# Kernel optimization log

Hardware: AMD Instinct MI355X
Metric: run time of the kernel (lower is better)

## Reference

```python
import jax, jax.numpy as jnp
import numpy as np

D_KEY = 128
INF = 1e9  # stands in for the module's global INF constant


def setup_inputs() -> dict:
    key = jax.random.key(0)
    kq, kk, kv = jax.random.split(key, 3)
    B, S, D = 8, 4096, D_KEY
    return {
        "query": jax.random.normal(kq, (B, S, D), dtype=jnp.float32),
        "keys": jax.random.normal(kk, (B, S, D), dtype=jnp.float32),
        "values": jax.random.normal(kv, (B, S, D), dtype=jnp.float32),
    }


def reference(query, keys, values):
    # dot_products: [B, Sq, Sk]
    scores = jnp.einsum("bqd,bkd->bqk", query, keys)
    S = scores.shape[-1]
    # causal: subtract INF on strict upper triangle (triu(1)), applied BEFORE scaling
    causal = jnp.triu(jnp.ones((S, S), dtype=scores.dtype), 1) * INF
    logits = (scores - causal[None, :, :]) / jnp.asarray(np.sqrt(D_KEY), scores.dtype)
    # legacy F.softmax on 3D transposed tensor == softmax over key axis
    probs = jax.nn.softmax(logits, axis=-1)
    # dropout with p=0.0 is identity
    return jnp.einsum("bqk,bkd->bqd", probs, values)
```

## Files before the change

kernel.cpp:

```cpp
#include <hip/hip_runtime.h>

#define B_SZ   8
#define S_LEN  4096
#define D_K    128
#define KB     64
#define CH     16
#define NCHUNK 640

#define PT_STR 72

typedef short  short8  __attribute__((ext_vector_type(8)));
typedef float  floatx4 __attribute__((ext_vector_type(4)));

#define EXP2F(x) exp2f(x)

__device__ __forceinline__ unsigned bfround(float x) {
  unsigned u = __builtin_bit_cast(unsigned, x);
  return (u + 0x7fffu + ((u >> 16) & 1u)) >> 16;
}
__device__ __forceinline__ unsigned bfpack2(float a, float b) {
  return bfround(a) | (bfround(b) << 16);
}
__device__ __forceinline__ unsigned cvtpk(float lo, float hi) {
  unsigned r;
  asm("v_cvt_pk_bf16_f32 %0, %1, %2" : "=v"(r) : "v"(lo), "v"(hi));
  return r;
}


__device__ __forceinline__ void dma16(const void* g, const void* l) {
  __builtin_amdgcn_global_load_lds(
      (__attribute__((address_space(1))) unsigned int*)(unsigned long long)g,
      (__attribute__((address_space(3))) unsigned int*)(unsigned int)(unsigned long long)l,
      16, 0, 0);
}


__global__ __launch_bounds__(256)
void prep(const float* __restrict__ K, const float* __restrict__ V,
          unsigned short* __restrict__ Kb, unsigned short* __restrict__ Vt,
          int* __restrict__ cnt) {
  __shared__ float tile[64][129];
  const int tid = threadIdx.x;
  const int bid = blockIdx.x;
  if (bid == 0 && tid == 0) *cnt = 0;
  const int b   = bid >> 6;
  const int s   = bid & 63;
  const int kt  = s * 64;

  {
    const int r  = tid >> 2;
    const int cq = tid & 3;
    const float* kp = K + (size_t)(b * S_LEN + kt + r) * D_K + cq * 32;
    unsigned short* kdst = Kb + (size_t)bid * 8192 + r * 128;
    const int xr = (r & 7) << 4;
#pragma unroll
    for (int jj = 0; jj < 4; ++jj) {
      float4 f0 = *(const float4*)(kp + jj * 8);
      float4 f1 = *(const float4*)(kp + jj * 8 + 4);
      uint4 u;
      u.x = bfpack2(f0.x, f0.y);
      u.y = bfpack2(f0.z, f0.w);
      u.z = bfpack2(f1.x, f1.y);
      u.w = bfpack2(f1.z, f1.w);
      const int o = (cq * 64 + jj * 16) ^ xr;
      *(uint4*)(kdst + (o >> 1)) = u;
    }
  }

  {
    const int k  = tid >> 2;
    const int cq = tid & 3;
    const float* vp = V + (size_t)(b * S_LEN + kt + k) * D_K + cq * 32;
#pragma unroll
    for (int i = 0; i < 8; ++i) {
      float4 f = *(const float4*)(vp + i * 4);
      tile[k][cq * 32 + i * 4]     = f.x;
      tile[k][cq * 32 + i * 4 + 1] = f.y;
      tile[k][cq * 32 + i * 4 + 2] = f.z;
      tile[k][cq * 32 + i * 4 + 3] = f.w;
    }
  }
  __syncthreads();

  {
    const int d = tid >> 1;
    const int h = tid & 1;
    unsigned short* vdst = Vt + (size_t)bid * 8192 + d * 64;
    const int xr = (d & 7) << 4;
#pragma unroll
    for (int jj = 0; jj < 4; ++jj) {
      const int k0 = h * 32 + jj * 8;
      uint4 u;
      u.x = bfpack2(tile[k0 + 0][d], tile[k0 + 1][d]);
      u.y = bfpack2(tile[k0 + 2][d], tile[k0 + 3][d]);
      u.z = bfpack2(tile[k0 + 4][d], tile[k0 + 5][d]);
      u.w = bfpack2(tile[k0 + 6][d], tile[k0 + 7][d]);
      const int o = (h * 64 + jj * 16) ^ xr;
      *(uint4*)(vdst + (o >> 1)) = u;
    }
  }
}


__global__ __launch_bounds__(256, 2)
void attn_worker(const float* __restrict__ Q, const unsigned short* __restrict__ Kb,
                 const unsigned short* __restrict__ Vt, int* __restrict__ cnt,
                 float* __restrict__ ml, float* __restrict__ pO) {
  __shared__ __align__(16) short Klds[2][8192];
  __shared__ __align__(16) short Vtlds[2][8192];
  __shared__ __align__(16) short Plds[4 * 16 * PT_STR];
  __shared__ int s_chunk;

  const int tid  = threadIdx.x;
  const int lane = tid & 63;
  const int w    = tid >> 6;
  const int l15  = lane & 15;
  const int quad = lane >> 4;
  const int xk   = (l15 & 7) << 3;

  const float CSC = 0.12752041f;

  for (;;) {
    if (tid == 0) s_chunk = atomicAdd(cnt, 1);
    __syncthreads();
    const int c = s_chunk;
    if (c >= NCHUNK) break;

    int b, q, j;
    if (c < 416) {
      const int r = c >> 3;  b = c & 7;
      if      (r <  4) { q = 31;              j = r;         }
      else if (r < 28) { q = 30 - (r-4)/3;    j = (r-4)%3;   }
      else if (r < 44) { q = 22 - (r-28)/2;   j = (r-28)%2;  }
      else             { q = 14 - (r-44);     j = 0;         }
    } else {
      const int rc = c - 416;
      const int g  = rc >> 5;
      const int t  = rc & 31;
      b = t & 7;
      q = (6 - g) + 8 * (3 - (t >> 3));
      j = (q + 1) >> 3;
    }

    const int q0 = q * 128;
    const int s0 = j * CH;
    const int s1 = min(s0 + CH, 2 * q + 2);

    short8 bq[2][4];
    int qg[2];
#pragma unroll
    for (int sub = 0; sub < 2; ++sub) {
      qg[sub] = q0 + w * 32 + sub * 16 + l15;
      const float* qrow = Q + (size_t)(b * S_LEN + qg[sub]) * D_K + quad * 8;
#pragma unroll
      for (int kd = 0; kd < 4; ++kd) {
        float4 f0 = *(const float4*)(qrow + kd * 32);
        float4 f1 = *(const float4*)(qrow + kd * 32 + 4);
        union { short8 s; unsigned u[4]; } t;
        t.u[0] = bfpack2(f0.x, f0.y);
        t.u[1] = bfpack2(f0.z, f0.w);
        t.u[2] = bfpack2(f1.x, f1.y);
        t.u[3] = bfpack2(f1.z, f1.w);
        bq[sub][kd] = t.s;
      }
    }

    floatx4 acc[2][8];
#pragma unroll
    for (int sub = 0; sub < 2; ++sub)
#pragma unroll
      for (int nc = 0; nc < 8; ++nc) acc[sub][nc] = (floatx4){0.f, 0.f, 0.f, 0.f};
    float m_run[2] = {-1e30f, -1e30f}, l_run[2] = {0.f, 0.f};

    const unsigned short* kb0 = Kb + (size_t)b * 64 * 8192;
    const unsigned short* vb0 = Vt + (size_t)b * 64 * 8192;
    const int lo = lane * 8;

#define STAGE(BUF, S)                                                          \
    do {                                                                       \
      const unsigned short* kg_ = kb0 + (size_t)(S) * 8192 + w * 2048 + lo;    \
      const unsigned short* vg_ = vb0 + (size_t)(S) * 8192 + w * 2048 + lo;    \
      short* kl_ = &Klds[BUF][w * 2048];                                       \
      short* vl_ = &Vtlds[BUF][w * 2048];                                      \
      _Pragma("unroll")                                                        \
      for (int i_ = 0; i_ < 4; ++i_) dma16(kg_ + i_ * 512, kl_ + i_ * 512);    \
      _Pragma("unroll")                                                        \
      for (int i_ = 0; i_ < 4; ++i_) dma16(vg_ + i_ * 512, vl_ + i_ * 512);    \
    } while (0)

    STAGE(s0 & 1, s0);
    if (s0 + 1 < s1) {
      STAGE((s0 + 1) & 1, s0 + 1);
      asm volatile("s_waitcnt vmcnt(8)" ::: "memory");
    } else {
      asm volatile("s_waitcnt vmcnt(0)" ::: "memory");
    }
    __builtin_amdgcn_s_barrier();
    __builtin_amdgcn_sched_barrier(0);

    for (int s = s0; s < s1; ++s) {
      const int kt  = s * KB;
      const int cur = s & 1;
      const short* Kl = &Klds[cur][0];
      const short* Vl = &Vtlds[cur][0];
      const bool act = (kt <= q0 + w * 32 + 31);

      short8 pa[2][2];
      if (act) {
        floatx4 st[2][4];
        __builtin_amdgcn_s_setprio(1);
#pragma unroll
        for (int kf = 0; kf < 4; ++kf) {
          floatx4 c0 = (floatx4){0.f, 0.f, 0.f, 0.f};
          floatx4 c1 = (floatx4){0.f, 0.f, 0.f, 0.f};
#pragma unroll
          for (int kd = 0; kd < 4; ++kd) {
            short8 a = *(const short8*)(&Kl[((kf * 16 + l15) << 7) + ((kd * 32 + quad * 8) ^ xk)]);
            c0 = __builtin_amdgcn_mfma_f32_16x16x32_bf16(a, bq[0][kd], c0, 0, 0, 0);
            c1 = __builtin_amdgcn_mfma_f32_16x16x32_bf16(a, bq[1][kd], c1, 0, 0, 0);
          }
          st[0][kf] = c0;
          st[1][kf] = c1;
        }
        __builtin_amdgcn_s_setprio(0);

#pragma unroll
        for (int sub = 0; sub < 2; ++sub) {
          if (kt + 63 > q0 + w * 32 + sub * 16) {
#pragma unroll
            for (int kf = 0; kf < 4; ++kf)
#pragma unroll
              for (int r = 0; r < 4; ++r) {
                int key = kt + kf * 16 + quad * 4 + r;
                if (key > qg[sub]) st[sub][kf][r] = -1e30f;
              }
          }
        }

#pragma unroll
        for (int sub = 0; sub < 2; ++sub) {
          float mx = st[sub][0][0];
#pragma unroll
          for (int kf = 0; kf < 4; ++kf)
#pragma unroll
            for (int r = 0; r < 4; ++r) mx = fmaxf(mx, st[sub][kf][r]);
          mx = fmaxf(mx, __shfl_xor(mx, 16, 64));
          mx = fmaxf(mx, __shfl_xor(mx, 32, 64));
          const float m_new = fmaxf(m_run[sub], mx);
          const bool  grow  = __any(m_new > m_run[sub]);

          float p[4][4];
          float tsum = 0.f;
#pragma unroll
          for (int kf = 0; kf < 4; ++kf)
#pragma unroll
            for (int r = 0; r < 4; ++r) {
              p[kf][r] = EXP2F((st[sub][kf][r] - m_new) * CSC);
              tsum += p[kf][r];
            }
          tsum += __shfl_xor(tsum, 16, 64);
          tsum += __shfl_xor(tsum, 32, 64);

          if (grow) {
            const float alpha = EXP2F((m_run[sub] - m_new) * CSC);
            l_run[sub] = l_run[sub] * alpha + tsum;
#pragma unroll
            for (int r = 0; r < 4; ++r) {
              const float ar = __shfl(alpha, quad * 4 + r, 64);
#pragma unroll
              for (int nc = 0; nc < 8; ++nc) acc[sub][nc][r] *= ar;
            }
          } else {
            l_run[sub] = l_run[sub] + tsum;
          }
          m_run[sub] = m_new;

          short* pw = &Plds[(w * 16 + l15) * PT_STR];
#pragma unroll
          for (int kf = 0; kf < 4; ++kf) {
            uint2 u;
            u.x = cvtpk(p[kf][0], p[kf][1]);
            u.y = cvtpk(p[kf][2], p[kf][3]);
            *(uint2*)(&pw[kf * 16 + quad * 4]) = u;
          }
          __asm__ __volatile__("" ::: "memory");
          pa[sub][0] = *(const short8*)(&pw[quad * 8]);
          pa[sub][1] = *(const short8*)(&pw[32 + quad * 8]);
          __asm__ __volatile__("" ::: "memory");
        }

        __builtin_amdgcn_s_setprio(1);
#pragma unroll
        for (int nc = 0; nc < 8; ++nc) {
          short8 bv0 = *(const short8*)(&Vl[((nc * 16 + l15) << 6) + ((quad * 8) ^ xk)]);
          short8 bv1 = *(const short8*)(&Vl[((nc * 16 + l15) << 6) + ((32 + quad * 8) ^ xk)]);
          acc[0][nc] = __builtin_amdgcn_mfma_f32_16x16x32_bf16(pa[0][0], bv0, acc[0][nc], 0, 0, 0);
          acc[0][nc] = __builtin_amdgcn_mfma_f32_16x16x32_bf16(pa[0][1], bv1, acc[0][nc], 0, 0, 0);
          acc[1][nc] = __builtin_amdgcn_mfma_f32_16x16x32_bf16(pa[1][0], bv0, acc[1][nc], 0, 0, 0);
          acc[1][nc] = __builtin_amdgcn_mfma_f32_16x16x32_bf16(pa[1][1], bv1, acc[1][nc], 0, 0, 0);
        }
        __builtin_amdgcn_s_setprio(0);
      }

      asm volatile("s_waitcnt lgkmcnt(0)" ::: "memory");
      __builtin_amdgcn_s_barrier();
      __builtin_amdgcn_sched_barrier(0);
      if (s + 2 < s1) {
        STAGE(cur, s + 2);
        asm volatile("s_waitcnt vmcnt(8)" ::: "memory");
      } else if (s + 1 < s1) {
        asm volatile("s_waitcnt vmcnt(0)" ::: "memory");
      }
      __builtin_amdgcn_s_barrier();
      __builtin_amdgcn_sched_barrier(0);
    }
#undef STAGE

    const int slot = ((b << 5) | q) * 4 + j;
    float* po = pO + (size_t)slot * 16384;
#pragma unroll
    for (int sub = 0; sub < 2; ++sub) {
#pragma unroll
      for (int r = 0; r < 4; ++r) {
        const int qrow = w * 32 + sub * 16 + quad * 4 + r;
        float* op = po + qrow * D_K + l15;
#pragma unroll
        for (int nc = 0; nc < 8; ++nc) op[nc * 16] = acc[sub][nc][r];
      }
      if (quad == 0) {
        const int qrow = w * 32 + sub * 16 + l15;
        ml[(size_t)slot * 256 + qrow * 2]     = m_run[sub];
        ml[(size_t)slot * 256 + qrow * 2 + 1] = l_run[sub];
      }
    }
  }
}


__global__ __launch_bounds__(256)
void attn_combine(const float* __restrict__ ml, const float* __restrict__ pO,
                  float* __restrict__ O) {
  const int t = blockIdx.x;
  const int b = t >> 5;
  const int q = t & 31;
  const int ncb = (2 * q + 17) >> 4;
  const float CSC = 0.12752041f;

  const int tid = threadIdx.x;
  const int ql  = tid >> 1;
  const int dh  = (tid & 1) * 64;

  float m[4], l[4], wgt[4];
  float M = -1e30f;
#pragma unroll
  for (int jj = 0; jj < 4; ++jj) {
    if (jj < ncb) {
      const int slot = t * 4 + jj;
      m[jj] = ml[(size_t)slot * 256 + ql * 2];
      l[jj] = ml[(size_t)slot * 256 + ql * 2 + 1];
      M = fmaxf(M, m[jj]);
    }
  }
  float L = 0.f;
#pragma unroll
  for (int jj = 0; jj < 4; ++jj)
    if (jj < ncb) { wgt[jj] = EXP2F((m[jj] - M) * CSC); L += wgt[jj] * l[jj]; }
  const float inv = 1.0f / L;

  float4 out[16];
#pragma unroll
  for (int v = 0; v < 16; ++v) out[v] = make_float4(0.f, 0.f, 0.f, 0.f);
#pragma unroll
  for (int jj = 0; jj < 4; ++jj) {
    if (jj < ncb) {
      const float* src = pO + (size_t)(t * 4 + jj) * 16384 + ql * D_K + dh;
      const float wj = wgt[jj];
#pragma unroll
      for (int v = 0; v < 16; ++v) {
        float4 f = *(const float4*)(src + v * 4);
        out[v].x += wj * f.x;  out[v].y += wj * f.y;
        out[v].z += wj * f.z;  out[v].w += wj * f.w;
      }
    }
  }
  float* dst = O + ((size_t)(b * S_LEN) + q * 128 + ql) * D_K + dh;
#pragma unroll
  for (int v = 0; v < 16; ++v) {
    *(float4*)(dst + v * 4) = make_float4(out[v].x * inv, out[v].y * inv,
                                          out[v].z * inv, out[v].w * inv);
  }
}


#define KT_STR 136
#define VT_STR 72

__global__ __launch_bounds__(256, 2)
void attn_fwd_fb(const float* __restrict__ Q, const float* __restrict__ K,
                 const float* __restrict__ V, float* __restrict__ O) {
  __shared__ __align__(16) short Klds[KB * KT_STR];
  __shared__ __align__(16) short Vtlds[D_K * VT_STR];
  __shared__ __align__(16) short Plds[4 * 16 * PT_STR];

  const int tid  = threadIdx.x;
  const int lane = tid & 63;
  const int w    = tid >> 6;
  const int l15  = lane & 15;
  const int quad = lane >> 4;

  const int bid = blockIdx.x;
  const int b   = bid & 7;
  const int qi  = 63 - (bid >> 3);
  const int q0  = qi * 64;

  const float CSC = 0.12752041f;

  const int    qg   = q0 + w * 16 + l15;
  const float* qrow = Q + (size_t)(b * S_LEN + qg) * D_K + quad * 8;
  short8 bq[4];
#pragma unroll
  for (int kd = 0; kd < 4; ++kd) {
    float4 f0 = *(const float4*)(qrow + kd * 32);
    float4 f1 = *(const float4*)(qrow + kd * 32 + 4);
    union { short8 s; unsigned u[4]; } t;
    t.u[0] = bfpack2(f0.x, f0.y);
    t.u[1] = bfpack2(f0.z, f0.w);
    t.u[2] = bfpack2(f1.x, f1.y);
    t.u[3] = bfpack2(f1.z, f1.w);
    bq[kd] = t.s;
  }

  floatx4 acc[8];
#pragma unroll
  for (int nc = 0; nc < 8; ++nc) acc[nc] = (floatx4){0.f, 0.f, 0.f, 0.f};
  float m_run = -1e30f, l_run = 0.f;

  const int d4 = tid & 31;
  const int kq = tid >> 5;
  const int nsteps = qi + 1;

  for (int s = 0; s < nsteps; ++s) {
    const int kt = s * KB;
#pragma unroll
    for (int r2 = 0; r2 < 2; ++r2) {
      const int row = r2 * 32 + kq * 4;
      const float* kp = K + (size_t)(b * S_LEN + kt + row) * D_K + d4 * 4;
      const float* vp = V + (size_t)(b * S_LEN + kt + row) * D_K + d4 * 4;
      float4 fk[4], fv[4];
#pragma unroll
      for (int i = 0; i < 4; ++i) {
        fk[i] = *(const float4*)(kp + i * D_K);
        fv[i] = *(const float4*)(vp + i * D_K);
      }
#pragma unroll
      for (int i = 0; i < 4; ++i) {
        uint2 u;
        u.x = bfpack2(fk[i].x, fk[i].y);
        u.y = bfpack2(fk[i].z, fk[i].w);
        *(uint2*)(&Klds[(row + i) * KT_STR + d4 * 4]) = u;
      }
#pragma unroll
      for (int c = 0; c < 4; ++c) {
        float e0 = ((const float*)&fv[0])[c];
        float e1 = ((const float*)&fv[1])[c];
        float e2 = ((const float*)&fv[2])[c];
        float e3 = ((const float*)&fv[3])[c];
        uint2 u;
        u.x = bfpack2(e0, e1);
        u.y = bfpack2(e2, e3);
        *(uint2*)(&Vtlds[(d4 * 4 + c) * VT_STR + row]) = u;
      }
    }
    __syncthreads();

    floatx4 st[4];
#pragma unroll
    for (int kf = 0; kf < 4; ++kf) {
      floatx4 cc = (floatx4){0.f, 0.f, 0.f, 0.f};
#pragma unroll
      for (int kd = 0; kd < 4; ++kd) {
        short8 a = *(const short8*)(&Klds[(kf * 16 + l15) * KT_STR + kd * 32 + quad * 8]);
        cc = __builtin_amdgcn_mfma_f32_16x16x32_bf16(a, bq[kd], cc, 0, 0, 0);
      }
      st[kf] = cc;
    }

    if (s == nsteps - 1) {
#pragma unroll
      for (int kf = 0; kf < 4; ++kf)
#pragma unroll
        for (int rr = 0; rr < 4; ++rr) {
          int key = kt + kf * 16 + quad * 4 + rr;
          if (key > qg) st[kf][rr] = -1e30f;
        }
    }

    float mx = st[0][0];
#pragma unroll
    for (int kf = 0; kf < 4; ++kf)
#pragma unroll
      for (int rr = 0; rr < 4; ++rr) mx = fmaxf(mx, st[kf][rr]);
    mx = fmaxf(mx, __shfl_xor(mx, 16, 64));
    mx = fmaxf(mx, __shfl_xor(mx, 32, 64));
    const float m_new = fmaxf(m_run, mx);
    const float alpha = EXP2F((m_run - m_new) * CSC);

    float p[4][4];
    float tsum = 0.f;
#pragma unroll
    for (int kf = 0; kf < 4; ++kf)
#pragma unroll
      for (int rr = 0; rr < 4; ++rr) {
        p[kf][rr] = EXP2F((st[kf][rr] - m_new) * CSC);
        tsum += p[kf][rr];
      }
    tsum += __shfl_xor(tsum, 16, 64);
    tsum += __shfl_xor(tsum, 32, 64);
    l_run = l_run * alpha + tsum;
    m_run = m_new;

#pragma unroll
    for (int rr = 0; rr < 4; ++rr) {
      const float ar = __shfl(alpha, quad * 4 + rr, 64);
#pragma unroll
      for (int nc = 0; nc < 8; ++nc) acc[nc][rr] *= ar;
    }

    short* pw = &Plds[(w * 16 + l15) * PT_STR];
#pragma unroll
    for (int kf = 0; kf < 4; ++kf) {
      uint2 u;
      u.x = bfpack2(p[kf][0], p[kf][1]);
      u.y = bfpack2(p[kf][2], p[kf][3]);
      *(uint2*)(&pw[kf * 16 + quad * 4]) = u;
    }
    __asm__ __volatile__("" ::: "memory");
    short8 pa0 = *(const short8*)(&pw[quad * 8]);
    short8 pa1 = *(const short8*)(&pw[32 + quad * 8]);

#pragma unroll
    for (int nc = 0; nc < 8; ++nc) {
      short8 bv0 = *(const short8*)(&Vtlds[(nc * 16 + l15) * VT_STR + quad * 8]);
      acc[nc] = __builtin_amdgcn_mfma_f32_16x16x32_bf16(pa0, bv0, acc[nc], 0, 0, 0);
      short8 bv1 = *(const short8*)(&Vtlds[(nc * 16 + l15) * VT_STR + 32 + quad * 8]);
      acc[nc] = __builtin_amdgcn_mfma_f32_16x16x32_bf16(pa1, bv1, acc[nc], 0, 0, 0);
    }
    __syncthreads();
  }

#pragma unroll
  for (int rr = 0; rr < 4; ++rr) {
    const float lr  = __shfl(l_run, quad * 4 + rr, 64);
    const float inv = 1.0f / lr;
    const int qout  = q0 + w * 16 + quad * 4 + rr;
    float* op = O + (size_t)(b * S_LEN + qout) * D_K + l15;
#pragma unroll
    for (int nc = 0; nc < 8; ++nc) op[nc * 16] = acc[nc][rr] * inv;
  }
}


extern "C" void kernel_launch(void* const* d_in, const int* in_sizes, int n_in,
                              void* d_out, int out_size, void* d_ws, size_t ws_size,
                              hipStream_t stream) {
  const float* Q = (const float*)d_in[0];
  const float* K = (const float*)d_in[1];
  const float* V = (const float*)d_in[2];
  float* O = (float*)d_out;

  const size_t elems = (size_t)B_SZ * S_LEN * D_K;

  const size_t off_ml = 256;
  const size_t off_po = off_ml + 1024ull * 256 * 4;
  const size_t off_kb = off_po + 1024ull * 16384 * 4;
  const size_t off_vt = off_kb + elems * 2;
  const size_t need   = off_vt + elems * 2;

  if (ws_size >= need) {
    char* ws = (char*)d_ws;
    int*            cnt = (int*)ws;
    float*          mlp = (float*)(ws + off_ml);
    float*          po  = (float*)(ws + off_po);
    unsigned short* Kbp = (unsigned short*)(ws + off_kb);
    unsigned short* Vtp = (unsigned short*)(ws + off_vt);

    prep<<<dim3(B_SZ * 64), dim3(256), 0, stream>>>(K, V, Kbp, Vtp, cnt);
    attn_worker<<<dim3(512), dim3(256), 0, stream>>>(Q, Kbp, Vtp, cnt, mlp, po);
    attn_combine<<<dim3(256), dim3(256), 0, stream>>>(mlp, po, O);
  } else {
    attn_fwd_fb<<<dim3(512), dim3(256), 0, stream>>>(Q, K, V, O);
  }
}
```

Baseline: 181.3 us.

## Replace atomic work queue with static 256-row 8-wave chunk schedule

Drops the persistent atomic-counter work loop and launches one 512-thread block per statically mapped chunk of 256 query rows by up to 8 key tiles, with balancing partial chunks for even tiles. The P staging buffer now reuses the current K LDS buffer after a barrier, which frees shared memory so more blocks can be resident. The combine kernel is rewritten for the new slot layout with up to 8 partials. This removes atomic and queue overhead and shares K/V staging across more query rows, at the cost of relying on a fixed schedule, which may balance less well, and adding an extra barrier per tile.

Measured after the change: 377.5 us. +108.2%, slower.

```diff
diff --git a/kernel.cpp b/kernel.cpp
--- a/kernel.cpp
+++ b/kernel.cpp
@@ -4,10 +4,8 @@
 #define S_LEN  4096
 #define D_K    128
 #define KB     64
-#define CH     16
-#define NCHUNK 640
-
-#define PT_STR 72
+#define NFULL  512
+#define NCHUNK 576
 
 typedef short  short8  __attribute__((ext_vector_type(8)));
 typedef float  floatx4 __attribute__((ext_vector_type(4)));
@@ -38,12 +36,10 @@
 
 __global__ __launch_bounds__(256)
 void prep(const float* __restrict__ K, const float* __restrict__ V,
-          unsigned short* __restrict__ Kb, unsigned short* __restrict__ Vt,
-          int* __restrict__ cnt) {
+          unsigned short* __restrict__ Kb, unsigned short* __restrict__ Vt) {
   __shared__ float tile[64][129];
   const int tid = threadIdx.x;
   const int bid = blockIdx.x;
-  if (bid == 0 && tid == 0) *cnt = 0;
   const int b   = bid >> 6;
   const int s   = bid & 63;
   const int kt  = s * 64;
@@ -103,14 +99,12 @@
 }
 
 
-__global__ __launch_bounds__(256, 2)
+__global__ __launch_bounds__(512, 4)
 void attn_worker(const float* __restrict__ Q, const unsigned short* __restrict__ Kb,
-                 const unsigned short* __restrict__ Vt, int* __restrict__ cnt,
+                 const unsigned short* __restrict__ Vt,
                  float* __restrict__ ml, float* __restrict__ pO) {
   __shared__ __align__(16) short Klds[2][8192];
   __shared__ __align__(16) short Vtlds[2][8192];
-  __shared__ __align__(16) short Plds[4 * 16 * PT_STR];
-  __shared__ int s_chunk;
 
   const int tid  = threadIdx.x;
   const int lane = tid & 63;
@@ -121,218 +115,211 @@
 
   const float CSC = 0.12752041f;
 
-  for (;;) {
-    if (tid == 0) s_chunk = atomicAdd(cnt, 1);
-    __syncthreads();
-    const int c = s_chunk;
-    if (c >= NCHUNK) break;
-
-    int b, q, j;
-    if (c < 416) {
-      const int r = c >> 3;  b = c & 7;
-      if      (r <  4) { q = 31;              j = r;         }
-      else if (r < 28) { q = 30 - (r-4)/3;    j = (r-4)%3;   }
-      else if (r < 44) { q = 22 - (r-28)/2;   j = (r-28)%2;  }
-      else             { q = 14 - (r-44);     j = 0;         }
-    } else {
-      const int rc = c - 416;
-      const int g  = rc >> 5;
-      const int t  = rc & 31;
-      b = t & 7;
-      q = (6 - g) + 8 * (3 - (t >> 3));
-      j = (q + 1) >> 3;
-    }
-
-    const int q0 = q * 128;
-    const int s0 = j * CH;
-    const int s1 = min(s0 + CH, 2 * q + 2);
-
-    short8 bq[2][4];
-    int qg[2];
-#pragma unroll
-    for (int sub = 0; sub < 2; ++sub) {
-      qg[sub] = q0 + w * 32 + sub * 16 + l15;
-      const float* qrow = Q + (size_t)(b * S_LEN + qg[sub]) * D_K + quad * 8;
-#pragma unroll
-      for (int kd = 0; kd < 4; ++kd) {
-        float4 f0 = *(const float4*)(qrow + kd * 32);
-        float4 f1 = *(const float4*)(qrow + kd * 32 + 4);
-        union { short8 s; unsigned u[4]; } t;
-        t.u[0] = bfpack2(f0.x, f0.y);
-        t.u[1] = bfpack2(f0.z, f0.w);
-        t.u[2] = bfpack2(f1.x, f1.y);
-        t.u[3] = bfpack2(f1.z, f1.w);
-        bq[sub][kd] = t.s;
-      }
-    }
-
-    floatx4 acc[2][8];
-#pragma unroll
-    for (int sub = 0; sub < 2; ++sub)
-#pragma unroll
-      for (int nc = 0; nc < 8; ++nc) acc[sub][nc] = (floatx4){0.f, 0.f, 0.f, 0.f};
-    float m_run[2] = {-1e30f, -1e30f}, l_run[2] = {0.f, 0.f};
-
-    const unsigned short* kb0 = Kb + (size_t)b * 64 * 8192;
-    const unsigned short* vb0 = Vt + (size_t)b * 64 * 8192;
-    const int lo = lane * 8;
+  const int orig = blockIdx.x;
+  const int wid  = (orig & 7) * 72 + (orig >> 3);
+
+  int b, t, s0, s1;
+  if (wid < NFULL) {
+    b = wid >> 6;
+    int r = wid & 63;
+    t = 15;
+    while (r >= ((t + 1) >> 1)) { r -= (t + 1) >> 1; --t; }
+    s0 = r * 8;  s1 = s0 + 8;
+  } else {
+    const int rc = wid - NFULL;
+    b = rc >> 3;
+    t = 14 - 2 * (rc & 7);
+    s0 = 4 * t;  s1 = s0 + 4;
+  }
+  const int q0 = t << 8;
+
+  short8 bq[2][4];
+  int qg[2];
+#pragma unroll
+  for (int sub = 0; sub < 2; ++sub) {
+    qg[sub] = q0 + w * 32 + sub * 16 + l15;
+    const float* qrow = Q + (size_t)(b * S_LEN + qg[sub]) * D_K + quad * 8;
+#pragma unroll
+    for (int kd = 0; kd < 4; ++kd) {
+      float4 f0 = *(const float4*)(qrow + kd * 32);
+      float4 f1 = *(const float4*)(qrow + kd * 32 + 4);
+      union { short8 s; unsigned u[4]; } tt;
+      tt.u[0] = bfpack2(f0.x, f0.y);
+      tt.u[1] = bfpack2(f0.z, f0.w);
+      tt.u[2] = bfpack2(f1.x, f1.y);
+      tt.u[3] = bfpack2(f1.z, f1.w);
+      bq[sub][kd] = tt.s;
+    }
+  }
+
+  floatx4 acc[2][8];
+#pragma unroll
+  for (int sub = 0; sub < 2; ++sub)
+#pragma unroll
+    for (int nc = 0; nc < 8; ++nc) acc[sub][nc] = (floatx4){0.f, 0.f, 0.f, 0.f};
+  float m_run[2] = {-1e30f, -1e30f}, l_run[2] = {0.f, 0.f};
+
+  const unsigned short* kb0 = Kb + (size_t)b * 64 * 8192;
+  const unsigned short* vb0 = Vt + (size_t)b * 64 * 8192;
+  const int lo = lane * 8;
 
 #define STAGE(BUF, S)                                                          \
-    do {                                                                       \
-      const unsigned short* kg_ = kb0 + (size_t)(S) * 8192 + w * 2048 + lo;    \
-      const unsigned short* vg_ = vb0 + (size_t)(S) * 8192 + w * 2048 + lo;    \
-      short* kl_ = &Klds[BUF][w * 2048];                                       \
-      short* vl_ = &Vtlds[BUF][w * 2048];                                      \
-      _Pragma("unroll")                                                        \
-      for (int i_ = 0; i_ < 4; ++i_) dma16(kg_ + i_ * 512, kl_ + i_ * 512);    \
-      _Pragma("unroll")                                                        \
-      for (int i_ = 0; i_ < 4; ++i_) dma16(vg_ + i_ * 512, vl_ + i_ * 512);    \
-    } while (0)
-
-    STAGE(s0 & 1, s0);
-    if (s0 + 1 < s1) {
-      STAGE((s0 + 1) & 1, s0 + 1);
-      asm volatile("s_waitcnt vmcnt(8)" ::: "memory");
-    } else {
-      asm volatile("s_waitcnt vmcnt(0)" ::: "memory");
-    }
+  do {                                                                         \
+    const unsigned short* kg_ = kb0 + (size_t)(S) * 8192 + w * 1024 + lo;      \
+    const unsigned short* vg_ = vb0 + (size_t)(S) * 8192 + w * 1024 + lo;      \
+    short* kl_ = &Klds[BUF][w * 1024];                                         \
+    short* vl_ = &Vtlds[BUF][w * 1024];                                        \
+    dma16(kg_, kl_);        dma16(kg_ + 512, kl_ + 512);                       \
+    dma16(vg_, vl_);        dma16(vg_ + 512, vl_ + 512);                       \
+  } while (0)
+
+  STAGE(s0 & 1, s0);
+  if (s0 + 1 < s1) {
+    STAGE((s0 + 1) & 1, s0 + 1);
+    asm volatile("s_waitcnt vmcnt(4)" ::: "memory");
+  } else {
+    asm volatile("s_waitcnt vmcnt(0)" ::: "memory");
+  }
+  __builtin_amdgcn_s_barrier();
+  __builtin_amdgcn_sched_barrier(0);
+
+  for (int s = s0; s < s1; ++s) {
+    const int kt  = s * KB;
+    const int cur = s & 1;
+    const short* Kl = &Klds[cur][0];
+    const short* Vl = &Vtlds[cur][0];
+    const bool act = (kt <= q0 + w * 32 + 31);
+
+    floatx4 st[2][4];
+    if (act) {
+      __builtin_amdgcn_s_setprio(1);
+#pragma unroll
+      for (int kf = 0; kf < 4; ++kf) {
+        floatx4 c0 = (floatx4){0.f, 0.f, 0.f, 0.f};
+        floatx4 c1 = (floatx4){0.f, 0.f, 0.f, 0.f};
+#pragma unroll
+        for (int kd = 0; kd < 4; ++kd) {
+          short8 a = *(const short8*)(&Kl[((kf * 16 + l15) << 7) + ((kd * 32 + quad * 8) ^ xk)]);
+          c0 = __builtin_amdgcn_mfma_f32_16x16x32_bf16(a, bq[0][kd], c0, 0, 0, 0);
+          c1 = __builtin_amdgcn_mfma_f32_16x16x32_bf16(a, bq[1][kd], c1, 0, 0, 0);
+        }
+        st[0][kf] = c0;
+        st[1][kf] = c1;
+      }
+      __builtin_amdgcn_s_setprio(0);
+
+#pragma unroll
+      for (int sub = 0; sub < 2; ++sub) {
+        if (kt + 63 > q0 + w * 32 + sub * 16) {
+#pragma unroll
+          for (int kf = 0; kf < 4; ++kf)
+#pragma unroll
+            for (int r = 0; r < 4; ++r) {
+              int key = kt + kf * 16 + quad * 4 + r;
+              if (key > qg[sub]) st[sub][kf][r] = -1e30f;
+            }
+        }
+      }
+    }
+
     __builtin_amdgcn_s_barrier();
     __builtin_amdgcn_sched_barrier(0);
 
-    for (int s = s0; s < s1; ++s) {
-      const int kt  = s * KB;
-      const int cur = s & 1;
-      const short* Kl = &Klds[cur][0];
-      const short* Vl = &Vtlds[cur][0];
-      const bool act = (kt <= q0 + w * 32 + 31);
-
-      short8 pa[2][2];
-      if (act) {
-        floatx4 st[2][4];
-        __builtin_amdgcn_s_setprio(1);
+    short8 pa[2][2];
+    if (act) {
+      short* pw = &Klds[cur][(w * 16 + l15) << 6];
+#pragma unroll
+      for (int sub = 0; sub < 2; ++sub) {
+        float mx = st[sub][0][0];
+#pragma unroll
+        for (int kf = 0; kf < 4; ++kf)
+#pragma unroll
+          for (int r = 0; r < 4; ++r) mx = fmaxf(mx, st[sub][kf][r]);
+        mx = fmaxf(mx, __shfl_xor(mx, 16, 64));
+        mx = fmaxf(mx, __shfl_xor(mx, 32, 64));
+        const float m_new = fmaxf(m_run[sub], mx);
+        const bool  grow  = __any(m_new > m_run[sub]);
+
+        float p[4][4];
+        float tsum = 0.f;
+#pragma unroll
+        for (int kf = 0; kf < 4; ++kf)
+#pragma unroll
+          for (int r = 0; r < 4; ++r) {
+            p[kf][r] = EXP2F((st[sub][kf][r] - m_new) * CSC);
+            tsum += p[kf][r];
+          }
+        tsum += __shfl_xor(tsum, 16, 64);
+        tsum += __shfl_xor(tsum, 32, 64);
+
+        if (grow) {
+          const float alpha = EXP2F((m_run[sub] - m_new) * CSC);
+          l_run[sub] = l_run[sub] * alpha + tsum;
+#pragma unroll
+          for (int r = 0; r < 4; ++r) {
+            const float ar = __shfl(alpha, quad * 4 + r, 64);
+#pragma unroll
+            for (int nc = 0; nc < 8; ++nc) acc[sub][nc][r] *= ar;
+          }
+        } else {
+          l_run[sub] = l_run[sub] + tsum;
+        }
+        m_run[sub] = m_new;
+
 #pragma unroll
         for (int kf = 0; kf < 4; ++kf) {
-          floatx4 c0 = (floatx4){0.f, 0.f, 0.f, 0.f};
-          floatx4 c1 = (floatx4){0.f, 0.f, 0.f, 0.f};
-#pragma unroll
-          for (int kd = 0; kd < 4; ++kd) {
-            short8 a = *(const short8*)(&Kl[((kf * 16 + l15) << 7) + ((kd * 32 + quad * 8) ^ xk)]);
-            c0 = __builtin_amdgcn_mfma_f32_16x16x32_bf16(a, bq[0][kd], c0, 0, 0, 0);
-            c1 = __builtin_amdgcn_mfma_f32_16x16x32_bf16(a, bq[1][kd], c1, 0, 0, 0);
-          }
-          st[0][kf] = c0;
-          st[1][kf] = c1;
+          uint2 u;
+          u.x = cvtpk(p[kf][0], p[kf][1]);
+          u.y = cvtpk(p[kf][2], p[kf][3]);
+          *(uint2*)(&pw[(kf * 16 + quad * 4) ^ xk]) = u;
         }
-        __builtin_amdgcn_s_setprio(0);
-
-#pragma unroll
-        for (int sub = 0; sub < 2; ++sub) {
-          if (kt + 63 > q0 + w * 32 + sub * 16) {
-#pragma unroll
-            for (int kf = 0; kf < 4; ++kf)
-#pragma unroll
-              for (int r = 0; r < 4; ++r) {
-                int key = kt + kf * 16 + quad * 4 + r;
-                if (key > qg[sub]) st[sub][kf][r] = -1e30f;
-              }
-          }
-        }
-
-#pragma unroll
-        for (int sub = 0; sub < 2; ++sub) {
-          float mx = st[sub][0][0];
-#pragma unroll
-          for (int kf = 0; kf < 4; ++kf)
-#pragma unroll
-            for (int r = 0; r < 4; ++r) mx = fmaxf(mx, st[sub][kf][r]);
-          mx = fmaxf(mx, __shfl_xor(mx, 16, 64));
-          mx = fmaxf(mx, __shfl_xor(mx, 32, 64));
-          const float m_new = fmaxf(m_run[sub], mx);
-          const bool  grow  = __any(m_new > m_run[sub]);
-
-          float p[4][4];
-          float tsum = 0.f;
-#pragma unroll
-          for (int kf = 0; kf < 4; ++kf)
-#pragma unroll
-            for (int r = 0; r < 4; ++r) {
-              p[kf][r] = EXP2F((st[sub][kf][r] - m_new) * CSC);
-              tsum += p[kf][r];
-            }
-          tsum += __shfl_xor(tsum, 16, 64);
-          tsum += __shfl_xor(tsum, 32, 64);
-
-          if (grow) {
-            const float alpha = EXP2F((m_run[sub] - m_new) * CSC);
-            l_run[sub] = l_run[sub] * alpha + tsum;
-#pragma unroll
-            for (int r = 0; r < 4; ++r) {
-              const float ar = __shfl(alpha, quad * 4 + r, 64);
-#pragma unroll
-              for (int nc = 0; nc < 8; ++nc) acc[sub][nc][r] *= ar;
-            }
-          } else {
-            l_run[sub] = l_run[sub] + tsum;
-          }
-          m_run[sub] = m_new;
-
-          short* pw = &Plds[(w * 16 + l15) * PT_STR];
-#pragma unroll
-          for (int kf = 0; kf < 4; ++kf) {
-            uint2 u;
-            u.x = cvtpk(p[kf][0], p[kf][1]);
-            u.y = cvtpk(p[kf][2], p[kf][3]);
-            *(uint2*)(&pw[kf * 16 + quad * 4]) = u;
-          }
-          __asm__ __volatile__("" ::: "memory");
-          pa[sub][0] = *(const short8*)(&pw[quad * 8]);
-          pa[sub][1] = *(const short8*)(&pw[32 + quad * 8]);
-          __asm__ __volatile__("" ::: "memory");
-        }
-
-        __builtin_amdgcn_s_setprio(1);
-#pragma unroll
-        for (int nc = 0; nc < 8; ++nc) {
-          short8 bv0 = *(const short8*)(&Vl[((nc * 16 + l15) << 6) + ((quad * 8) ^ xk)]);
-          short8 bv1 = *(const short8*)(&Vl[((nc * 16 + l15) << 6) + ((32 + quad * 8) ^ xk)]);
-          acc[0][nc] = __builtin_amdgcn_mfma_f32_16x16x32_bf16(pa[0][0], bv0, acc[0][nc], 0, 0, 0);
-          acc[0][nc] = __builtin_amdgcn_mfma_f32_16x16x32_bf16(pa[0][1], bv1, acc[0][nc], 0, 0, 0);
-          acc[1][nc] = __builtin_amdgcn_mfma_f32_16x16x32_bf16(pa[1][0], bv0, acc[1][nc], 0, 0, 0);
-          acc[1][nc] = __builtin_amdgcn_mfma_f32_16x16x32_bf16(pa[1][1], bv1, acc[1][nc], 0, 0, 0);
-        }
-        __builtin_amdgcn_s_setprio(0);
-      }
-
-      asm volatile("s_waitcnt lgkmcnt(0)" ::: "memory");
-      __builtin_amdgcn_s_barrier();
-      __builtin_amdgcn_sched_barrier(0);
-      if (s + 2 < s1) {
-        STAGE(cur, s + 2);
-        asm volatile("s_waitcnt vmcnt(8)" ::: "memory");
-      } else if (s + 1 < s1) {
-        asm volatile("s_waitcnt vmcnt(0)" ::: "memory");
-      }
-      __builtin_amdgcn_s_barrier();
-      __builtin_amdgcn_sched_barrier(0);
-    }
+        __asm__ __volatile__("" ::: "memory");
+        pa[sub][0] = *(const short8*)(&pw[(quad * 8) ^ xk]);
+        pa[sub][1] = *(const short8*)(&pw[(32 + quad * 8) ^ xk]);
+        __asm__ __volatile__("" ::: "memory");
+      }
+
+      __builtin_amdgcn_s_setprio(1);
+#pragma unroll
+      for (int nc = 0; nc < 8; ++nc) {
+        short8 bv0 = *(const short8*)(&Vl[((nc * 16 + l15) << 6) + ((quad * 8) ^ xk)]);
+        short8 bv1 = *(const short8*)(&Vl[((nc * 16 + l15) << 6) + ((32 + quad * 8) ^ xk)]);
+        acc[0][nc] = __builtin_amdgcn_mfma_f32_16x16x32_bf16(pa[0][0], bv0, acc[0][nc], 0, 0, 0);
+        acc[0][nc] = __builtin_amdgcn_mfma_f32_16x16x32_bf16(pa[0][1], bv1, acc[0][nc], 0, 0, 0);
+        acc[1][nc] = __builtin_amdgcn_mfma_f32_16x16x32_bf16(pa[1][0], bv0, acc[1][nc], 0, 0, 0);
+        acc[1][nc] = __builtin_amdgcn_mfma_f32_16x16x32_bf16(pa[1][1], bv1, acc[1][nc], 0, 0, 0);
+      }
+      __builtin_amdgcn_s_setprio(0);
+    }
+
+    asm volatile("s_waitcnt lgkmcnt(0)" ::: "memory");
+    __builtin_amdgcn_s_barrier();
+    __builtin_amdgcn_sched_barrier(0);
+    if (s + 2 < s1) {
+      STAGE(cur, s + 2);
+      asm volatile("s_waitcnt vmcnt(4)" ::: "memory");
+    } else if (s + 1 < s1) {
+      asm volatile("s_waitcnt vmcnt(0)" ::: "memory");
+    }
+    __builtin_amdgcn_s_barrier();
+    __builtin_amdgcn_sched_barrier(0);
+  }
 #undef STAGE
 
-    const int slot = ((b << 5) | q) * 4 + j;
-    float* po = pO + (size_t)slot * 16384;
-#pragma unroll
-    for (int sub = 0; sub < 2; ++sub) {
-#pragma unroll
-      for (int r = 0; r < 4; ++r) {
-        const int qrow = w * 32 + sub * 16 + quad * 4 + r;
-        float* op = po + qrow * D_K + l15;
-#pragma unroll
-        for (int nc = 0; nc < 8; ++nc) op[nc * 16] = acc[sub][nc][r];
-      }
-      if (quad == 0) {
-        const int qrow = w * 32 + sub * 16 + l15;
-        ml[(size_t)slot * 256 + qrow * 2]     = m_run[sub];
-        ml[(size_t)slot * 256 + qrow * 2 + 1] = l_run[sub];
-      }
+  float* po = pO + (size_t)wid * 32768;
+#pragma unroll
+  for (int sub = 0; sub < 2; ++sub) {
+#pragma unroll
+    for (int r = 0; r < 4; ++r) {
+      const int qrow = w * 32 + sub * 16 + quad * 4 + r;
+      float* op = po + qrow * D_K + l15;
+#pragma unroll
+      for (int nc = 0; nc < 8; ++nc) op[nc * 16] = acc[sub][nc][r];
+    }
+    if (quad == 0) {
+      const int qrow = w * 32 + sub * 16 + l15;
+      ml[(size_t)wid * 512 + qrow * 2]     = m_run[sub];
+      ml[(size_t)wid * 512 + qrow * 2 + 1] = l_run[sub];
     }
   }
 }
@@ -341,41 +328,50 @@
 __global__ __launch_bounds__(256)
 void attn_combine(const float* __restrict__ ml, const float* __restrict__ pO,
                   float* __restrict__ O) {
-  const int t = blockIdx.x;
-  const int b = t >> 5;
-  const int q = t & 31;
-  const int ncb = (2 * q + 17) >> 4;
+  const int cb   = blockIdx.x;
+  const int half = cb & 1;
+  const int bt   = cb >> 1;
+  const int b    = bt >> 4;
+  const int t    = bt & 15;
   const float CSC = 0.12752041f;
 
-  const int tid = threadIdx.x;
-  const int ql  = tid >> 1;
-  const int dh  = (tid & 1) * 64;
-
-  float m[4], l[4], wgt[4];
+  const int q  = threadIdx.x;
+  const int dh = half * 64;
+
+  int cum = 0;
+  for (int tt = 15; tt > t; --tt) cum += (tt + 1) >> 1;
+  const int nf = (t + 1) >> 1;
+  int slots[8];
+  int ns = 0;
+#pragma unroll
+  for (int jj = 0; jj < 8; ++jj)
+    if (jj < nf) { slots[ns] = b * 64 + cum + jj; ++ns; }
+  if (!(t & 1)) { slots[ns] = NFULL + b * 8 + (7 - (t >> 1)); ++ns; }
+
+  float m[8], l[8], wgt[8];
   float M = -1e30f;
 #pragma unroll
-  for (int jj = 0; jj < 4; ++jj) {
-    if (jj < ncb) {
-      const int slot = t * 4 + jj;
-      m[jj] = ml[(size_t)slot * 256 + ql * 2];
-      l[jj] = ml[(size_t)slot * 256 + ql * 2 + 1];
-      M = fmaxf(M, m[jj]);
+  for (int i = 0; i < 8; ++i) {
+    if (i < ns) {
+      m[i] = ml[(size_t)slots[i] * 512 + q * 2];
+      l[i] = ml[(size_t)slots[i] * 512 + q * 2 + 1];
+      M = fmaxf(M, m[i]);
     }
   }
   float L = 0.f;
 #pragma unroll
-  for (int jj = 0; jj < 4; ++jj)
-    if (jj < ncb) { wgt[jj] = EXP2F((m[jj] - M) * CSC); L += wgt[jj] * l[jj]; }
+  for (int i = 0; i < 8; ++i)
+    if (i < ns) { wgt[i] = EXP2F((m[i] - M) * CSC); L += wgt[i] * l[i]; }
   const float inv = 1.0f / L;
 
   float4 out[16];
 #pragma unroll
   for (int v = 0; v < 16; ++v) out[v] = make_float4(0.f, 0.f, 0.f, 0.f);
 #pragma unroll
-  for (int jj = 0; jj < 4; ++jj) {
-    if (jj < ncb) {
-      const float* src = pO + (size_t)(t * 4 + jj) * 16384 + ql * D_K + dh;
-      const float wj = wgt[jj];
+  for (int i = 0; i < 8; ++i) {
+    if (i < ns) {
+      const float* src = pO + (size_t)slots[i] * 32768 + q * D_K + dh;
+      const float wj = wgt[i];
 #pragma unroll
       for (int v = 0; v < 16; ++v) {
         float4 f = *(const float4*)(src + v * 4);
@@ -384,7 +380,7 @@
       }
     }
   }
-  float* dst = O + ((size_t)(b * S_LEN) + q * 128 + ql) * D_K + dh;
+  float* dst = O + ((size_t)(b * S_LEN) + t * 256 + q) * D_K + dh;
 #pragma unroll
   for (int v = 0; v < 16; ++v) {
     *(float4*)(dst + v * 4) = make_float4(out[v].x * inv, out[v].y * inv,
@@ -395,6 +391,7 @@
 
 #define KT_STR 136
 #define VT_STR 72
+#define PT_STR 72
 
 __global__ __launch_bounds__(256, 2)
 void attn_fwd_fb(const float* __restrict__ Q, const float* __restrict__ K,
@@ -571,22 +568,21 @@
 
   const size_t elems = (size_t)B_SZ * S_LEN * D_K;
 
-  const size_t off_ml = 256;
-  const size_t off_po = off_ml + 1024ull * 256 * 4;
-  const size_t off_kb = off_po + 1024ull * 16384 * 4;
+  const size_t off_ml = 0;
+  const size_t off_po = (size_t)NCHUNK * 512 * 4;
+  const size_t off_kb = off_po + (size_t)NCHUNK * 32768 * 4;
   const size_t off_vt = off_kb + elems * 2;
   const size_t need   = off_vt + elems * 2;
 
   if (ws_size >= need) {
     char* ws = (char*)d_ws;
-    int*            cnt = (int*)ws;
     float*          mlp = (float*)(ws + off_ml);
     float*          po  = (float*)(ws + off_po);
     unsigned short* Kbp = (unsigned short*)(ws + off_kb);
     unsigned short* Vtp = (unsigned short*)(ws + off_vt);
 
-    prep<<<dim3(B_SZ * 64), dim3(256), 0, stream>>>(K, V, Kbp, Vtp, cnt);
-    attn_worker<<<dim3(512), dim3(256), 0, stream>>>(Q, Kbp, Vtp, cnt, mlp, po);
+    prep<<<dim3(B_SZ * 64), dim3(256), 0, stream>>>(K, V, Kbp, Vtp);
+    attn_worker<<<dim3(NCHUNK), dim3(512), 0, stream>>>(Q, Kbp, Vtp, mlp, po);
     attn_combine<<<dim3(256), dim3(256), 0, stream>>>(mlp, po, O);
   } else {
     attn_fwd_fb<<<dim3(512), dim3(256), 0, stream>>>(Q, K, V, O);
```

## Shrink LDS footprint for three blocks per CU with finer split-K chunks

Applied to the files above, without the earlier changes.

The worker now keeps a single V buffer instead of two, writes P into the consumed K buffer, and drops the separate P scratch area. With less LDS per block it raises launch bounds to three blocks per CU and launches 768 persistent blocks. Chunks shrink from 16 to 8 key tiles, with a generic loop mapping chunk to (q, j), and the combine kernel now merges up to 8 partials. Fast exp2 is also used. In exchange there is an extra barrier and vmcnt(0) wait per tile, V loads are no longer double-buffered, and more partial results must be written and combined.

Measured after the change: 238.6 us. 31.6% more time.

```diff
diff --git a/kernel.cpp b/kernel.cpp
--- a/kernel.cpp
+++ b/kernel.cpp
@@ -4,15 +4,21 @@
 #define S_LEN  4096
 #define D_K    128
 #define KB     64
-#define CH     16
-#define NCHUNK 640
-
-#define PT_STR 72
+#define CH     8
+#define NCHUNK 1152
+#define NC(q)  (((q) + 4) >> 2)
 
 typedef short  short8  __attribute__((ext_vector_type(8)));
 typedef float  floatx4 __attribute__((ext_vector_type(4)));
 
+#if defined(__has_builtin)
+#if __has_builtin(__builtin_amdgcn_exp2f)
+#define EXP2F(x) __builtin_amdgcn_exp2f(x)
+#endif
+#endif
+#ifndef EXP2F
 #define EXP2F(x) exp2f(x)
+#endif
 
 __device__ __forceinline__ unsigned bfround(float x) {
   unsigned u = __builtin_bit_cast(unsigned, x);
@@ -103,13 +109,12 @@
 }
 
 
-__global__ __launch_bounds__(256, 2)
+__global__ __launch_bounds__(256, 3)
 void attn_worker(const float* __restrict__ Q, const unsigned short* __restrict__ Kb,
                  const unsigned short* __restrict__ Vt, int* __restrict__ cnt,
                  float* __restrict__ ml, float* __restrict__ pO) {
   __shared__ __align__(16) short Klds[2][8192];
-  __shared__ __align__(16) short Vtlds[2][8192];
-  __shared__ __align__(16) short Plds[4 * 16 * PT_STR];
+  __shared__ __align__(16) short Vtlds[8192];
   __shared__ int s_chunk;
 
   const int tid  = threadIdx.x;
@@ -127,22 +132,10 @@
     const int c = s_chunk;
     if (c >= NCHUNK) break;
 
-    int b, q, j;
-    if (c < 416) {
-      const int r = c >> 3;  b = c & 7;
-      if      (r <  4) { q = 31;              j = r;         }
-      else if (r < 28) { q = 30 - (r-4)/3;    j = (r-4)%3;   }
-      else if (r < 44) { q = 22 - (r-28)/2;   j = (r-28)%2;  }
-      else             { q = 14 - (r-44);     j = 0;         }
-    } else {
-      const int rc = c - 416;
-      const int g  = rc >> 5;
-      const int t  = rc & 31;
-      b = t & 7;
-      q = (6 - g) + 8 * (3 - (t >> 3));
-      j = (q + 1) >> 3;
-    }
-
+    const int b = c & 7;
+    int q = 31, r = c >> 3;
+    while (r >= NC(q)) { r -= NC(q); --q; }
+    const int j  = r;
     const int q0 = q * 128;
     const int s0 = j * CH;
     const int s1 = min(s0 + CH, 2 * q + 2);
@@ -157,12 +150,12 @@
       for (int kd = 0; kd < 4; ++kd) {
         float4 f0 = *(const float4*)(qrow + kd * 32);
         float4 f1 = *(const float4*)(qrow + kd * 32 + 4);
-        union { short8 s; unsigned u[4]; } t;
-        t.u[0] = bfpack2(f0.x, f0.y);
-        t.u[1] = bfpack2(f0.z, f0.w);
-        t.u[2] = bfpack2(f1.x, f1.y);
-        t.u[3] = bfpack2(f1.z, f1.w);
-        bq[sub][kd] = t.s;
+        union { short8 s; unsigned u[4]; } tt;
+        tt.u[0] = bfpack2(f0.x, f0.y);
+        tt.u[1] = bfpack2(f0.z, f0.w);
+        tt.u[2] = bfpack2(f1.x, f1.y);
+        tt.u[3] = bfpack2(f1.z, f1.w);
+        bq[sub][kd] = tt.s;
       }
     }
 
@@ -177,25 +170,25 @@
     const unsigned short* vb0 = Vt + (size_t)b * 64 * 8192;
     const int lo = lane * 8;
 
-#define STAGE(BUF, S)                                                          \
+#define STAGE_K(BUF, S)                                                        \
     do {                                                                       \
       const unsigned short* kg_ = kb0 + (size_t)(S) * 8192 + w * 2048 + lo;    \
-      const unsigned short* vg_ = vb0 + (size_t)(S) * 8192 + w * 2048 + lo;    \
       short* kl_ = &Klds[BUF][w * 2048];                                       \
-      short* vl_ = &Vtlds[BUF][w * 2048];                                      \
       _Pragma("unroll")                                                        \
       for (int i_ = 0; i_ < 4; ++i_) dma16(kg_ + i_ * 512, kl_ + i_ * 512);    \
+    } while (0)
+#define STAGE_V(S)                                                             \
+    do {                                                                       \
+      const unsigned short* vg_ = vb0 + (size_t)(S) * 8192 + w * 2048 + lo;    \
+      short* vl_ = &Vtlds[w * 2048];                                           \
       _Pragma("unroll")                                                        \
       for (int i_ = 0; i_ < 4; ++i_) dma16(vg_ + i_ * 512, vl_ + i_ * 512);    \
     } while (0)
 
-    STAGE(s0 & 1, s0);
-    if (s0 + 1 < s1) {
-      STAGE((s0 + 1) & 1, s0 + 1);
-      asm volatile("s_waitcnt vmcnt(8)" ::: "memory");
-    } else {
-      asm volatile("s_waitcnt vmcnt(0)" ::: "memory");
-    }
+    STAGE_K(s0 & 1, s0);
+    if (s0 + 1 < s1) STAGE_K((s0 + 1) & 1, s0 + 1);
+    STAGE_V(s0);
+    asm volatile("s_waitcnt vmcnt(0)" ::: "memory");
     __builtin_amdgcn_s_barrier();
     __builtin_amdgcn_sched_barrier(0);
 
@@ -203,12 +196,10 @@
       const int kt  = s * KB;
       const int cur = s & 1;
       const short* Kl = &Klds[cur][0];
-      const short* Vl = &Vtlds[cur][0];
       const bool act = (kt <= q0 + w * 32 + 31);
 
-      short8 pa[2][2];
+      floatx4 st[2][4];
       if (act) {
-        floatx4 st[2][4];
         __builtin_amdgcn_s_setprio(1);
 #pragma unroll
         for (int kf = 0; kf < 4; ++kf) {
@@ -231,20 +222,28 @@
 #pragma unroll
             for (int kf = 0; kf < 4; ++kf)
 #pragma unroll
-              for (int r = 0; r < 4; ++r) {
-                int key = kt + kf * 16 + quad * 4 + r;
-                if (key > qg[sub]) st[sub][kf][r] = -1e30f;
+              for (int rr = 0; rr < 4; ++rr) {
+                int key = kt + kf * 16 + quad * 4 + rr;
+                if (key > qg[sub]) st[sub][kf][rr] = -1e30f;
               }
           }
         }
-
+      }
+
+      asm volatile("s_waitcnt vmcnt(0)" ::: "memory");
+      __builtin_amdgcn_s_barrier();
+      __builtin_amdgcn_sched_barrier(0);
+
+      short8 pa[2][2];
+      if (act) {
+        short* pw = &Klds[cur][(w * 16 + l15) << 6];
 #pragma unroll
         for (int sub = 0; sub < 2; ++sub) {
           float mx = st[sub][0][0];
 #pragma unroll
           for (int kf = 0; kf < 4; ++kf)
 #pragma unroll
-            for (int r = 0; r < 4; ++r) mx = fmaxf(mx, st[sub][kf][r]);
+            for (int rr = 0; rr < 4; ++rr) mx = fmaxf(mx, st[sub][kf][rr]);
           mx = fmaxf(mx, __shfl_xor(mx, 16, 64));
           mx = fmaxf(mx, __shfl_xor(mx, 32, 64));
           const float m_new = fmaxf(m_run[sub], mx);
@@ -255,9 +254,9 @@
 #pragma unroll
           for (int kf = 0; kf < 4; ++kf)
 #pragma unroll
-            for (int r = 0; r < 4; ++r) {
-              p[kf][r] = EXP2F((st[sub][kf][r] - m_new) * CSC);
-              tsum += p[kf][r];
+            for (int rr = 0; rr < 4; ++rr) {
+              p[kf][rr] = EXP2F((st[sub][kf][rr] - m_new) * CSC);
+              tsum += p[kf][rr];
             }
           tsum += __shfl_xor(tsum, 16, 64);
           tsum += __shfl_xor(tsum, 32, 64);
@@ -266,35 +265,34 @@
             const float alpha = EXP2F((m_run[sub] - m_new) * CSC);
             l_run[sub] = l_run[sub] * alpha + tsum;
 #pragma unroll
-            for (int r = 0; r < 4; ++r) {
-              const float ar = __shfl(alpha, quad * 4 + r, 64);
-#pragma unroll
-              for (int nc = 0; nc < 8; ++nc) acc[sub][nc][r] *= ar;
+            for (int rr = 0; rr < 4; ++rr) {
+              const float ar = __shfl(alpha, quad * 4 + rr, 64);
+#pragma unroll
+              for (int nc = 0; nc < 8; ++nc) acc[sub][nc][rr] *= ar;
             }
           } else {
             l_run[sub] = l_run[sub] + tsum;
           }
           m_run[sub] = m_new;
 
-          short* pw = &Plds[(w * 16 + l15) * PT_STR];
 #pragma unroll
           for (int kf = 0; kf < 4; ++kf) {
             uint2 u;
             u.x = cvtpk(p[kf][0], p[kf][1]);
             u.y = cvtpk(p[kf][2], p[kf][3]);
-            *(uint2*)(&pw[kf * 16 + quad * 4]) = u;
+            *(uint2*)(&pw[(kf * 16 + quad * 4) ^ xk]) = u;
           }
           __asm__ __volatile__("" ::: "memory");
-          pa[sub][0] = *(const short8*)(&pw[quad * 8]);
-          pa[sub][1] = *(const short8*)(&pw[32 + quad * 8]);
+          pa[sub][0] = *(const short8*)(&pw[(quad * 8) ^ xk]);
+          pa[sub][1] = *(const short8*)(&pw[(32 + quad * 8) ^ xk]);
           __asm__ __volatile__("" ::: "memory");
         }
 
         __builtin_amdgcn_s_setprio(1);
 #pragma unroll
         for (int nc = 0; nc < 8; ++nc) {
-          short8 bv0 = *(const short8*)(&Vl[((nc * 16 + l15) << 6) + ((quad * 8) ^ xk)]);
-          short8 bv1 = *(const short8*)(&Vl[((nc * 16 + l15) << 6) + ((32 + quad * 8) ^ xk)]);
+          short8 bv0 = *(const short8*)(&Vtlds[((nc * 16 + l15) << 6) + ((quad * 8) ^ xk)]);
+          short8 bv1 = *(const short8*)(&Vtlds[((nc * 16 + l15) << 6) + ((32 + quad * 8) ^ xk)]);
           acc[0][nc] = __builtin_amdgcn_mfma_f32_16x16x32_bf16(pa[0][0], bv0, acc[0][nc], 0, 0, 0);
           acc[0][nc] = __builtin_amdgcn_mfma_f32_16x16x32_bf16(pa[0][1], bv1, acc[0][nc], 0, 0, 0);
           acc[1][nc] = __builtin_amdgcn_mfma_f32_16x16x32_bf16(pa[1][0], bv0, acc[1][nc], 0, 0, 0);
@@ -306,32 +304,26 @@
       asm volatile("s_waitcnt lgkmcnt(0)" ::: "memory");
       __builtin_amdgcn_s_barrier();
       __builtin_amdgcn_sched_barrier(0);
-      if (s + 2 < s1) {
-        STAGE(cur, s + 2);
-        asm volatile("s_waitcnt vmcnt(8)" ::: "memory");
-      } else if (s + 1 < s1) {
-        asm volatile("s_waitcnt vmcnt(0)" ::: "memory");
-      }
-      __builtin_amdgcn_s_barrier();
-      __builtin_amdgcn_sched_barrier(0);
-    }
-#undef STAGE
-
-    const int slot = ((b << 5) | q) * 4 + j;
-    float* po = pO + (size_t)slot * 16384;
+      if (s + 2 < s1) STAGE_K(cur, s + 2);
+      if (s + 1 < s1) STAGE_V(s + 1);
+    }
+#undef STAGE_K
+#undef STAGE_V
+
+    float* po = pO + (size_t)c * 16384;
 #pragma unroll
     for (int sub = 0; sub < 2; ++sub) {
 #pragma unroll
-      for (int r = 0; r < 4; ++r) {
-        const int qrow = w * 32 + sub * 16 + quad * 4 + r;
+      for (int rr = 0; rr < 4; ++rr) {
+        const int qrow = w * 32 + sub * 16 + quad * 4 + rr;
         float* op = po + qrow * D_K + l15;
 #pragma unroll
-        for (int nc = 0; nc < 8; ++nc) op[nc * 16] = acc[sub][nc][r];
+        for (int nc = 0; nc < 8; ++nc) op[nc * 16] = acc[sub][nc][rr];
       }
       if (quad == 0) {
         const int qrow = w * 32 + sub * 16 + l15;
-        ml[(size_t)slot * 256 + qrow * 2]     = m_run[sub];
-        ml[(size_t)slot * 256 + qrow * 2 + 1] = l_run[sub];
+        ml[(size_t)c * 256 + qrow * 2]     = m_run[sub];
+        ml[(size_t)c * 256 + qrow * 2 + 1] = l_run[sub];
       }
     }
   }
@@ -344,38 +336,42 @@
   const int t = blockIdx.x;
   const int b = t >> 5;
   const int q = t & 31;
-  const int ncb = (2 * q + 17) >> 4;
   const float CSC = 0.12752041f;
 
   const int tid = threadIdx.x;
   const int ql  = tid >> 1;
   const int dh  = (tid & 1) * 64;
 
-  float m[4], l[4], wgt[4];
+  int cum = 0;
+  for (int tq = 31; tq > q; --tq) cum += NC(tq);
+  const int ncb = NC(q);
+
+  float m[8], l[8], wgt[8];
   float M = -1e30f;
 #pragma unroll
-  for (int jj = 0; jj < 4; ++jj) {
-    if (jj < ncb) {
-      const int slot = t * 4 + jj;
-      m[jj] = ml[(size_t)slot * 256 + ql * 2];
-      l[jj] = ml[(size_t)slot * 256 + ql * 2 + 1];
-      M = fmaxf(M, m[jj]);
+  for (int i = 0; i < 8; ++i) {
+    if (i < ncb) {
+      const size_t slot = (size_t)((cum + i) << 3 | b);
+      m[i] = ml[slot * 256 + ql * 2];
+      l[i] = ml[slot * 256 + ql * 2 + 1];
+      M = fmaxf(M, m[i]);
     }
   }
   float L = 0.f;
 #pragma unroll
-  for (int jj = 0; jj < 4; ++jj)
-    if (jj < ncb) { wgt[jj] = EXP2F((m[jj] - M) * CSC); L += wgt[jj] * l[jj]; }
+  for (int i = 0; i < 8; ++i)
+    if (i < ncb) { wgt[i] = EXP2F((m[i] - M) * CSC); L += wgt[i] * l[i]; }
   const float inv = 1.0f / L;
 
   float4 out[16];
 #pragma unroll
   for (int v = 0; v < 16; ++v) out[v] = make_float4(0.f, 0.f, 0.f, 0.f);
 #pragma unroll
-  for (int jj = 0; jj < 4; ++jj) {
-    if (jj < ncb) {
-      const float* src = pO + (size_t)(t * 4 + jj) * 16384 + ql * D_K + dh;
-      const float wj = wgt[jj];
+  for (int i = 0; i < 8; ++i) {
+    if (i < ncb) {
+      const size_t slot = (size_t)((cum + i) << 3 | b);
+      const float* src = pO + slot * 16384 + ql * D_K + dh;
+      const float wj = wgt[i];
 #pragma unroll
       for (int v = 0; v < 16; ++v) {
         float4 f = *(const float4*)(src + v * 4);
@@ -395,6 +391,7 @@
 
 #define KT_STR 136
 #define VT_STR 72
+#define PT_STR 72
 
 __global__ __launch_bounds__(256, 2)
 void attn_fwd_fb(const float* __restrict__ Q, const float* __restrict__ K,
@@ -572,8 +569,8 @@
   const size_t elems = (size_t)B_SZ * S_LEN * D_K;
 
   const size_t off_ml = 256;
-  const size_t off_po = off_ml + 1024ull * 256 * 4;
-  const size_t off_kb = off_po + 1024ull * 16384 * 4;
+  const size_t off_po = off_ml + (size_t)NCHUNK * 256 * 4;
+  const size_t off_kb = off_po + (size_t)NCHUNK * 16384 * 4;
   const size_t off_vt = off_kb + elems * 2;
   const size_t need   = off_vt + elems * 2;
 
@@ -586,7 +583,7 @@
     unsigned short* Vtp = (unsigned short*)(ws + off_vt);
 
     prep<<<dim3(B_SZ * 64), dim3(256), 0, stream>>>(K, V, Kbp, Vtp, cnt);
-    attn_worker<<<dim3(512), dim3(256), 0, stream>>>(Q, Kbp, Vtp, cnt, mlp, po);
+    attn_worker<<<dim3(768), dim3(256), 0, stream>>>(Q, Kbp, Vtp, cnt, mlp, po);
     attn_combine<<<dim3(256), dim3(256), 0, stream>>>(mlp, po, O);
   } else {
     attn_fwd_fb<<<dim3(512), dim3(256), 0, stream>>>(Q, K, V, O);
```
